# Optimization experiments

Hardware: AMD Instinct MI355X
Metric: run time of the kernel (lower is better)

The kernel has to match this reference:

```python
import jax, jax.numpy as jnp
import numpy as np

DK = 64
DROPOUT_P = 0.1


def setup_inputs() -> dict:
    key = jax.random.key(0)
    kq, kk, kv, km = jax.random.split(key, 4)
    B, S, D = 16, 2048, 64
    q = jax.random.normal(kq, (B, S, D), dtype=jnp.float32)
    k = jax.random.normal(kk, (B, S, D), dtype=jnp.float32)
    v = jax.random.normal(kv, (B, S, D), dtype=jnp.float32)
    attn_mask = jax.random.randint(km, (S, S), 0, 2, dtype=jnp.int32)
    return {"q": q, "k": k, "v": v, "attn_mask": attn_mask}


def reference(q, k, v, attn_mask):
    # q = q / sqrt(dk)
    qs = q * (1.0 / np.sqrt(DK)).astype(np.float32)
    # dots: [B, S_q, S_k]
    dots = jnp.einsum("bqd,bkd->bqk", qs, k)
    # mask: 0 -> -inf, 1 -> 0 (additive)
    add_mask = jnp.where(attn_mask == 0, -jnp.inf, 0.0).astype(dots.dtype)
    dots = dots + add_mask  # broadcast [S,S] over batch
    attn = jax.nn.softmax(dots, axis=-1)
    # inverted dropout, train mode, fixed key for determinism
    keep = jax.random.bernoulli(jax.random.key(42), 1.0 - DROPOUT_P, attn.shape)
    attn = jnp.where(keep, attn * (1.0 / (1.0 - DROPOUT_P)), 0.0)
    out = jnp.einsum("bqk,bkd->bqd", attn, v)
    return out
```

## Files before the change

### kernel.cpp

```cpp
#include <hip/hip_runtime.h>

#define BATCH 16
#define SEQ   2048
#define DIM   64
#define NTHREADS 256

typedef short bf16x8 __attribute__((ext_vector_type(8)));
typedef float f32x4 __attribute__((ext_vector_type(4)));

__device__ __forceinline__ int ldsoff(int row) {
  return row * 72 + 16 * (row >> 2);
}
#define LDS_SZ (64 * 72 + 16 * 16)

__device__ __forceinline__ unsigned tf_bits(unsigned f) {
  unsigned x0 = 0u;
  unsigned x1 = f;
  const unsigned ks1 = 42u;
  const unsigned ks2 = 0x1BD11BDAu ^ 42u;
  x1 += ks1;
#define TF_R(r) { x0 += x1; x1 = __builtin_amdgcn_alignbit(x1, x1, 32u - (r)); x1 ^= x0; }
  TF_R(13) TF_R(15) TF_R(26) TF_R(6)
  x0 += ks1; x1 += ks2 + 1u;
  TF_R(17) TF_R(29) TF_R(16) TF_R(24)
  x0 += ks2; x1 += 2u;
  TF_R(13) TF_R(15) TF_R(26) TF_R(6)
  x1 += ks1 + 3u;
  TF_R(17) TF_R(29) TF_R(16) TF_R(24)
  x0 += ks1; x1 += ks2 + 4u;
  TF_R(13) TF_R(15) TF_R(26) TF_R(6)
  x0 += ks2; x1 += 5u;
#undef TF_R
  return x0 ^ x1;
}
#define KEEP_THRESH 0xE6666600u

__device__ __forceinline__ unsigned pack_bf16x2(float lo, float hi) {
  const unsigned l = (__float_as_uint(lo) + 0x8000u) >> 16;
  const unsigned h = (__float_as_uint(hi) + 0x8000u) & 0xFFFF0000u;
  return h | l;
}
__device__ __forceinline__ unsigned pack_trunc(float lo, float hi) {
  return __builtin_amdgcn_perm(__float_as_uint(hi), __float_as_uint(lo), 0x07060302u);
}
__device__ __forceinline__ unsigned cvtpk(float lo, float hi) {
  unsigned r;
  asm("v_cvt_pk_bf16_f32 %0, %1, %2" : "=v"(r) : "v"(lo), "v"(hi));
  return r;
}

#define WS_KF 0
#define WS_VF 1048576
#define WS_MB 2097152
#define WS_O0 2228224
#define WS_L  4325376

__global__ __launch_bounds__(NTHREADS)
void prep(const float* __restrict__ k, const float* __restrict__ v,
          const int* __restrict__ mask, unsigned* __restrict__ ws) {
  __shared__ float TS[64 * 68];
  const int t = threadIdx.x;
  const unsigned bx = blockIdx.x;

  if (bx < 1024) {
    const int x  = (int)bx & 7;
    const int j  = (int)bx >> 3;
    const int b  = 2 * x + (j & 1);
    const int j2 = j >> 1;
    const int kt = j2 & 31;
    const int kv = j2 >> 5;
    const float* src = (kv ? v : k) + ((size_t)b * SEQ + kt * 64) * DIM;

#pragma unroll
    for (int s = 0; s < 4; ++s) {
      const int row = s * 16 + (t >> 4);
      const int c4  = (t & 15) * 4;
      *(float4*)&TS[row * 68 + c4] = *(const float4*)(src + (size_t)row * DIM + c4);
    }
    __syncthreads();

    const int lane = t & 63, tx = lane & 15, quad = lane >> 4, sub = t >> 6;
    if (kv == 0) {
#pragma unroll
      for (int i = 0; i < 2; ++i) {
        const int combo = sub * 2 + i, nt = combo >> 1, ks = combo & 1;
        const float* rp = &TS[(4 * tx + nt) * 68 + ks * 32 + quad * 8];
        const float4 f0 = *(const float4*)rp;
        const float4 f1 = *(const float4*)(rp + 4);
        uint4 wout;
        wout.x = cvtpk(f0.x, f0.y); wout.y = cvtpk(f0.z, f0.w);
        wout.z = cvtpk(f1.x, f1.y); wout.w = cvtpk(f1.z, f1.w);
        const unsigned e = ((((unsigned)b * 32 + kt) * 4 + nt) * 2 + ks) * 64 + lane;
        *(uint4*)(ws + WS_KF + (size_t)e * 4) = wout;
      }
    } else {
#pragma unroll
      for (int i = 0; i < 2; ++i) {
        const int combo = sub * 2 + i, nt = combo >> 1, ks = combo & 1;
        const float* cp = &TS[(ks * 32 + quad * 8) * 68 + nt * 16 + tx];
        uint4 wout;
        wout.x = cvtpk(cp[0 * 68], cp[1 * 68]);
        wout.y = cvtpk(cp[2 * 68], cp[3 * 68]);
        wout.z = cvtpk(cp[4 * 68], cp[5 * 68]);
        wout.w = cvtpk(cp[6 * 68], cp[7 * 68]);
        const unsigned e = ((((unsigned)b * 32 + kt) * 4 + nt) * 2 + ks) * 64 + lane;
        *(uint4*)(ws + WS_VF + (size_t)e * 4) = wout;
      }
    }
    return;
  }

  const unsigned pid = (bx - 1024u) * NTHREADS + (unsigned)t;
  const unsigned C4 = pid & 511u, R4 = pid >> 9;
  unsigned m16 = 0u;
#pragma unroll
  for (int rr = 0; rr < 4; ++rr) {
    const int4 mv = *(const int4*)(mask + (size_t)(4 * R4 + rr) * SEQ + 4 * C4);
    m16 |= (mv.x ? 1u : 0u) << (rr * 4 + 0);
    m16 |= (mv.y ? 1u : 0u) << (rr * 4 + 1);
    m16 |= (mv.z ? 1u : 0u) << (rr * 4 + 2);
    m16 |= (mv.w ? 1u : 0u) << (rr * 4 + 3);
  }
  ((unsigned short*)(ws + WS_MB))[pid] = (unsigned short)m16;
}

__global__ __launch_bounds__(NTHREADS, 4)
void attn_fwd(const float* __restrict__ q, const unsigned* __restrict__ ws,
              float* __restrict__ out) {
  __shared__ unsigned short PS[LDS_SZ];

  const int t    = threadIdx.x;
  const int w    = t >> 6;
  const int lane = t & 63;
  const int tx   = lane & 15;
  const int quad = lane >> 4;

  const int x  = (int)blockIdx.x & 7;
  const int j  = (int)blockIdx.x >> 3;
  const int bb = 2 * x + (j & 1);
  const int j2 = j >> 1;
  const int q0 = (j2 & 31) * 64;
  const int sk = j2 >> 5;
  const int qw = q0 + 16 * w;
  const int kt0 = sk * 16;

  const float qscale = 0.125f * 1.44269504088896340736f;

  bf16x8 aq[2];
  {
    const float* qr = q + ((size_t)bb * SEQ + qw + tx) * DIM + quad * 8;
#pragma unroll
    for (int ks = 0; ks < 2; ++ks) {
      const float4 f0 = *(const float4*)(qr + ks * 32);
      const float4 f1 = *(const float4*)(qr + ks * 32 + 4);
      union { unsigned u[4]; bf16x8 v; } a;
      a.u[0] = pack_bf16x2(f0.x * qscale, f0.y * qscale);
      a.u[1] = pack_bf16x2(f0.z * qscale, f0.w * qscale);
      a.u[2] = pack_bf16x2(f1.x * qscale, f1.y * qscale);
      a.u[3] = pack_bf16x2(f1.z * qscale, f1.w * qscale);
      aq[ks] = a.v;
    }
  }

  float lrun[4] = {0.f, 0.f, 0.f, 0.f};
  f32x4 oacc[4];
#pragma unroll
  for (int nt = 0; nt < 4; ++nt) oacc[nt] = (f32x4){0.f, 0.f, 0.f, 0.f};

  const unsigned* kfb = ws + WS_KF + (size_t)(bb * 32) * 2048 + (size_t)lane * 4;
  const unsigned* vfb = ws + WS_VF + (size_t)(bb * 32) * 2048 + (size_t)lane * 4;
  const unsigned short* maskp = (const unsigned short*)(ws + WS_MB)
      + ((size_t)((qw >> 2) + quad)) * 512 + tx;
  const unsigned fbase0 = (unsigned)(bb * SEQ + qw + quad * 4) * (unsigned)SEQ
                          + (unsigned)(4 * tx);

  bf16x8 vf[4][2];

#define RNG_PWRITE(kt_, qk_, mw_)                                              \
  {                                                                            \
    const unsigned fb = fbase0 + (unsigned)((kt_) * 64);                       \
    _Pragma("unroll")                                                          \
    for (int reg = 0; reg < 4; ++reg) {                                        \
      const unsigned mnib = (mw_) >> (reg * 4);                                \
      float pd[4];                                                             \
      float ls = 0.0f;                                                         \
      _Pragma("unroll")                                                        \
      for (int nt = 0; nt < 4; ++nt) {                                         \
        const float s = (mnib & (1u << nt)) ? qk_[nt][reg] : -1e30f;           \
        const float e = __builtin_amdgcn_exp2f(s);                             \
        ls += e;                                                               \
        const unsigned bits = tf_bits(fb + (unsigned)(reg * SEQ) + (unsigned)nt); \
        pd[nt] = (bits < KEEP_THRESH) ? e : 0.0f;                              \
      }                                                                        \
      lrun[reg] += ls;                                                         \
      uint2 pw;                                                                \
      pw.x = pack_trunc(pd[0], pd[1]);                                         \
      pw.y = pack_trunc(pd[2], pd[3]);                                         \
      *(uint2*)&PS[ldsoff(16 * w + quad * 4 + reg) + 4 * tx] = pw;             \
    }                                                                          \
  }

#define LOAD_KF(kt_)                                                           \
    const unsigned* kfp = kfb + (size_t)(kt_) * 2048;                          \
    bf16x8 kf[4][2];                                                           \
    _Pragma("unroll")                                                          \
    for (int nt = 0; nt < 4; ++nt)                                             \
      _Pragma("unroll")                                                        \
      for (int ks = 0; ks < 2; ++ks)                                           \
        kf[nt][ks] = *(const bf16x8*)(kfp + (nt * 2 + ks) * 256);

#define PV_STEP                                                                \
    _Pragma("unroll")                                                          \
    for (int ks = 0; ks < 2; ++ks) {                                           \
      const bf16x8 ap = *(const bf16x8*)&PS[ldsoff(16 * w + tx) + ks * 32 + quad * 8]; \
      _Pragma("unroll")                                                        \
      for (int nt = 0; nt < 4; ++nt)                                           \
        oacc[nt] = __builtin_amdgcn_mfma_f32_16x16x32_bf16(ap, vf[nt][ks],     \
                                                           oacc[nt], 0, 0, 0); \
    }

#define LOAD_VF(kt_)                                                           \
    const unsigned* vfp = vfb + (size_t)(kt_) * 2048;                          \
    _Pragma("unroll")                                                          \
    for (int nt = 0; nt < 4; ++nt)                                             \
      _Pragma("unroll")                                                        \
      for (int ks = 0; ks < 2; ++ks)                                           \
        vf[nt][ks] = *(const bf16x8*)(vfp + (nt * 2 + ks) * 256);

#define QK_STEP(qk_)                                                           \
    f32x4 qk_[4];                                                              \
    _Pragma("unroll")                                                          \
    for (int nt = 0; nt < 4; ++nt) {                                           \
      f32x4 c = (f32x4){0.f, 0.f, 0.f, 0.f};                                   \
      _Pragma("unroll")                                                        \
      for (int ks = 0; ks < 2; ++ks)                                           \
        c = __builtin_amdgcn_mfma_f32_16x16x32_bf16(aq[ks], kf[nt][ks], c, 0, 0, 0); \
      qk_[nt] = c;                                                             \
    }

  {
    LOAD_KF(kt0)
    LOAD_VF(kt0)
    const unsigned mwv = maskp[kt0 * 16];
    QK_STEP(qk)
    RNG_PWRITE(kt0, qk, mwv)
  }
#pragma unroll 1
  for (int kt = kt0 + 1; kt < kt0 + 16; ++kt) {
    LOAD_KF(kt)
    const unsigned mwv = maskp[kt * 16];
    PV_STEP
    LOAD_VF(kt)
    QK_STEP(qk)
    RNG_PWRITE(kt, qk, mwv)
  }
  PV_STEP

  float lsum[4];
#pragma unroll
  for (int reg = 0; reg < 4; ++reg) {
    float ls = lrun[reg];
    ls += __shfl_xor(ls, 1);
    ls += __shfl_xor(ls, 2);
    ls += __shfl_xor(ls, 4);
    ls += __shfl_xor(ls, 8);
    lsum[reg] = ls;
  }
  float* wsf = (float*)ws;
  const size_t off = ((size_t)bb * SEQ + qw) * DIM;
  float* ob = sk ? out + off : wsf + WS_O0 + off;
#pragma unroll
  for (int nt = 0; nt < 4; ++nt)
#pragma unroll
    for (int reg = 0; reg < 4; ++reg)
      ob[(size_t)(quad * 4 + reg) * DIM + nt * 16 + tx] = oacc[nt][reg];
  if (tx == 0) {
    float* lp = wsf + WS_L + sk * 32768 + bb * SEQ + qw + quad * 4;
#pragma unroll
    for (int reg = 0; reg < 4; ++reg) lp[reg] = lsum[reg];
  }
}

__global__ __launch_bounds__(NTHREADS)
void combine(float* __restrict__ out, const unsigned* __restrict__ ws) {
  const unsigned gid = blockIdx.x * NTHREADS + threadIdx.x;
  const float* wsf = (const float*)ws;
  const float4 a = ((const float4*)out)[gid];
  const float4 b = ((const float4*)(wsf + WS_O0))[gid];
  const unsigned row = gid >> 4;
  const float linv = (1.0f / 0.9f) / (wsf[WS_L + row] + wsf[WS_L + 32768u + row]);
  float4 o;
  o.x = (a.x + b.x) * linv;
  o.y = (a.y + b.y) * linv;
  o.z = (a.z + b.z) * linv;
  o.w = (a.w + b.w) * linv;
  ((float4*)out)[gid] = o;
}

extern "C" void kernel_launch(void* const* d_in, const int* in_sizes, int n_in,
                              void* d_out, int out_size, void* d_ws, size_t ws_size,
                              hipStream_t stream) {
  const float* q = (const float*)d_in[0];
  const float* k = (const float*)d_in[1];
  const float* v = (const float*)d_in[2];
  const int* mask = (const int*)d_in[3];
  float* out = (float*)d_out;
  unsigned* ws = (unsigned*)d_ws;

  hipLaunchKernelGGL(prep, dim3(2048), dim3(NTHREADS), 0, stream,
                     k, v, mask, ws);
  hipLaunchKernelGGL(attn_fwd, dim3(1024), dim3(NTHREADS), 0, stream,
                     q, ws, out);
  hipLaunchKernelGGL(combine, dim3(2048), dim3(NTHREADS), 0, stream, out, ws);
}
```

Measured before the change: 225.7 us.

## Fuse prep and combine into single attention kernel with in-block split-K reduction

```diff
diff --git a/kernel.cpp b/kernel.cpp
--- a/kernel.cpp
+++ b/kernel.cpp
@@ -49,100 +49,26 @@
   return r;
 }
 
-#define WS_KF 0
-#define WS_VF 1048576
-#define WS_MB 2097152
-#define WS_O0 2228224
-#define WS_L  4325376
-
-__global__ __launch_bounds__(NTHREADS)
-void prep(const float* __restrict__ k, const float* __restrict__ v,
-          const int* __restrict__ mask, unsigned* __restrict__ ws) {
-  __shared__ float TS[64 * 68];
-  const int t = threadIdx.x;
-  const unsigned bx = blockIdx.x;
-
-  if (bx < 1024) {
-    const int x  = (int)bx & 7;
-    const int j  = (int)bx >> 3;
-    const int b  = 2 * x + (j & 1);
-    const int j2 = j >> 1;
-    const int kt = j2 & 31;
-    const int kv = j2 >> 5;
-    const float* src = (kv ? v : k) + ((size_t)b * SEQ + kt * 64) * DIM;
-
-#pragma unroll
-    for (int s = 0; s < 4; ++s) {
-      const int row = s * 16 + (t >> 4);
-      const int c4  = (t & 15) * 4;
-      *(float4*)&TS[row * 68 + c4] = *(const float4*)(src + (size_t)row * DIM + c4);
-    }
-    __syncthreads();
-
-    const int lane = t & 63, tx = lane & 15, quad = lane >> 4, sub = t >> 6;
-    if (kv == 0) {
-#pragma unroll
-      for (int i = 0; i < 2; ++i) {
-        const int combo = sub * 2 + i, nt = combo >> 1, ks = combo & 1;
-        const float* rp = &TS[(4 * tx + nt) * 68 + ks * 32 + quad * 8];
-        const float4 f0 = *(const float4*)rp;
-        const float4 f1 = *(const float4*)(rp + 4);
-        uint4 wout;
-        wout.x = cvtpk(f0.x, f0.y); wout.y = cvtpk(f0.z, f0.w);
-        wout.z = cvtpk(f1.x, f1.y); wout.w = cvtpk(f1.z, f1.w);
-        const unsigned e = ((((unsigned)b * 32 + kt) * 4 + nt) * 2 + ks) * 64 + lane;
-        *(uint4*)(ws + WS_KF + (size_t)e * 4) = wout;
-      }
-    } else {
-#pragma unroll
-      for (int i = 0; i < 2; ++i) {
-        const int combo = sub * 2 + i, nt = combo >> 1, ks = combo & 1;
-        const float* cp = &TS[(ks * 32 + quad * 8) * 68 + nt * 16 + tx];
-        uint4 wout;
-        wout.x = cvtpk(cp[0 * 68], cp[1 * 68]);
-        wout.y = cvtpk(cp[2 * 68], cp[3 * 68]);
-        wout.z = cvtpk(cp[4 * 68], cp[5 * 68]);
-        wout.w = cvtpk(cp[6 * 68], cp[7 * 68]);
-        const unsigned e = ((((unsigned)b * 32 + kt) * 4 + nt) * 2 + ks) * 64 + lane;
-        *(uint4*)(ws + WS_VF + (size_t)e * 4) = wout;
-      }
-    }
-    return;
-  }
-
-  const unsigned pid = (bx - 1024u) * NTHREADS + (unsigned)t;
-  const unsigned C4 = pid & 511u, R4 = pid >> 9;
-  unsigned m16 = 0u;
-#pragma unroll
-  for (int rr = 0; rr < 4; ++rr) {
-    const int4 mv = *(const int4*)(mask + (size_t)(4 * R4 + rr) * SEQ + 4 * C4);
-    m16 |= (mv.x ? 1u : 0u) << (rr * 4 + 0);
-    m16 |= (mv.y ? 1u : 0u) << (rr * 4 + 1);
-    m16 |= (mv.z ? 1u : 0u) << (rr * 4 + 2);
-    m16 |= (mv.w ? 1u : 0u) << (rr * 4 + 3);
-  }
-  ((unsigned short*)(ws + WS_MB))[pid] = (unsigned short)m16;
-}
-
 __global__ __launch_bounds__(NTHREADS, 4)
-void attn_fwd(const float* __restrict__ q, const unsigned* __restrict__ ws,
+void attn_all(const float* __restrict__ q, const float* __restrict__ k,
+              const float* __restrict__ v, const int* __restrict__ mask,
               float* __restrict__ out) {
-  __shared__ unsigned short PS[LDS_SZ];
+  __shared__ __align__(16) unsigned short PS[LDS_SZ];
 
   const int t    = threadIdx.x;
   const int w    = t >> 6;
   const int lane = t & 63;
   const int tx   = lane & 15;
   const int quad = lane >> 4;
+  const int rh   = w & 1;
+  const int kh   = w >> 1;
 
   const int x  = (int)blockIdx.x & 7;
   const int j  = (int)blockIdx.x >> 3;
   const int bb = 2 * x + (j & 1);
-  const int j2 = j >> 1;
-  const int q0 = (j2 & 31) * 64;
-  const int sk = j2 >> 5;
-  const int qw = q0 + 16 * w;
-  const int kt0 = sk * 16;
+  const int qb = (j >> 1) * 32;
+  const int qw = qb + 16 * rh;
+  const int kt0 = kh * 16;
 
   const float qscale = 0.125f * 1.44269504088896340736f;
 
@@ -167,26 +93,83 @@
 #pragma unroll
   for (int nt = 0; nt < 4; ++nt) oacc[nt] = (f32x4){0.f, 0.f, 0.f, 0.f};
 
-  const unsigned* kfb = ws + WS_KF + (size_t)(bb * 32) * 2048 + (size_t)lane * 4;
-  const unsigned* vfb = ws + WS_VF + (size_t)(bb * 32) * 2048 + (size_t)lane * 4;
-  const unsigned short* maskp = (const unsigned short*)(ws + WS_MB)
-      + ((size_t)((qw >> 2) + quad)) * 512 + tx;
+  const float* kb = k + (size_t)bb * SEQ * DIM;
+  const float* vb = v + (size_t)bb * SEQ * DIM;
+  const int* mrow = mask + (size_t)(qw + quad * 4) * SEQ + 4 * tx;
   const unsigned fbase0 = (unsigned)(bb * SEQ + qw + quad * 4) * (unsigned)SEQ
                           + (unsigned)(4 * tx);
 
   bf16x8 vf[4][2];
 
-#define RNG_PWRITE(kt_, qk_, mw_)                                              \
+#define LOAD_KF(kt_)                                                           \
+    bf16x8 kf[4][2];                                                           \
+    _Pragma("unroll")                                                          \
+    for (int nt = 0; nt < 4; ++nt)                                             \
+      _Pragma("unroll")                                                        \
+      for (int ks = 0; ks < 2; ++ks) {                                         \
+        const float* rp = kb + (size_t)((kt_) * 64 + 4 * tx + nt) * DIM        \
+                             + ks * 32 + quad * 8;                             \
+        const float4 f0 = *(const float4*)rp;                                  \
+        const float4 f1 = *(const float4*)(rp + 4);                            \
+        union { unsigned u[4]; bf16x8 v; } c;                                  \
+        c.u[0] = cvtpk(f0.x, f0.y); c.u[1] = cvtpk(f0.z, f0.w);                \
+        c.u[2] = cvtpk(f1.x, f1.y); c.u[3] = cvtpk(f1.z, f1.w);                \
+        kf[nt][ks] = c.v;                                                      \
+      }
+
+#define LOAD_VF(kt_)                                                           \
+    _Pragma("unroll")                                                          \
+    for (int nt = 0; nt < 4; ++nt)                                             \
+      _Pragma("unroll")                                                        \
+      for (int ks = 0; ks < 2; ++ks) {                                         \
+        const float* cp = vb + (size_t)((kt_) * 64 + ks * 32 + quad * 8) * DIM \
+                             + nt * 16 + tx;                                   \
+        union { unsigned u[4]; bf16x8 v; } c;                                  \
+        c.u[0] = cvtpk(cp[0 * DIM], cp[1 * DIM]);                              \
+        c.u[1] = cvtpk(cp[2 * DIM], cp[3 * DIM]);                              \
+        c.u[2] = cvtpk(cp[4 * DIM], cp[5 * DIM]);                              \
+        c.u[3] = cvtpk(cp[6 * DIM], cp[7 * DIM]);                              \
+        vf[nt][ks] = c.v;                                                      \
+      }
+
+#define LOAD_MASK(kt_, mv_)                                                    \
+    int4 mv_[4];                                                               \
+    _Pragma("unroll")                                                          \
+    for (int reg = 0; reg < 4; ++reg)                                          \
+      mv_[reg] = *(const int4*)(mrow + (size_t)reg * SEQ + (kt_) * 64);
+
+#define PV_STEP                                                                \
+    _Pragma("unroll")                                                          \
+    for (int ks = 0; ks < 2; ++ks) {                                           \
+      const bf16x8 ap = *(const bf16x8*)&PS[ldsoff(16 * w + tx) + ks * 32 + quad * 8]; \
+      _Pragma("unroll")                                                        \
+      for (int nt = 0; nt < 4; ++nt)                                           \
+        oacc[nt] = __builtin_amdgcn_mfma_f32_16x16x32_bf16(ap, vf[nt][ks],     \
+                                                           oacc[nt], 0, 0, 0); \
+    }
+
+#define QK_STEP(qk_)                                                           \
+    f32x4 qk_[4];                                                              \
+    _Pragma("unroll")                                                          \
+    for (int nt = 0; nt < 4; ++nt) {                                           \
+      f32x4 c = (f32x4){0.f, 0.f, 0.f, 0.f};                                   \
+      _Pragma("unroll")                                                        \
+      for (int ks = 0; ks < 2; ++ks)                                           \
+        c = __builtin_amdgcn_mfma_f32_16x16x32_bf16(aq[ks], kf[nt][ks], c, 0, 0, 0); \
+      qk_[nt] = c;                                                             \
+    }
+
+#define RNG_PWRITE(kt_, qk_, mv_)                                              \
   {                                                                            \
     const unsigned fb = fbase0 + (unsigned)((kt_) * 64);                       \
     _Pragma("unroll")                                                          \
     for (int reg = 0; reg < 4; ++reg) {                                        \
-      const unsigned mnib = (mw_) >> (reg * 4);                                \
+      const int* mr = (const int*)&mv_[reg];                                   \
       float pd[4];                                                             \
       float ls = 0.0f;                                                         \
       _Pragma("unroll")                                                        \
       for (int nt = 0; nt < 4; ++nt) {                                         \
-        const float s = (mnib & (1u << nt)) ? qk_[nt][reg] : -1e30f;           \
+        const float s = mr[nt] ? qk_[nt][reg] : -1e30f;                        \
         const float e = __builtin_amdgcn_exp2f(s);                             \
         ls += e;                                                               \
         const unsigned bits = tf_bits(fb + (unsigned)(reg * SEQ) + (unsigned)nt); \
@@ -200,59 +183,21 @@
     }                                                                          \
   }
 
-#define LOAD_KF(kt_)                                                           \
-    const unsigned* kfp = kfb + (size_t)(kt_) * 2048;                          \
-    bf16x8 kf[4][2];                                                           \
-    _Pragma("unroll")                                                          \
-    for (int nt = 0; nt < 4; ++nt)                                             \
-      _Pragma("unroll")                                                        \
-      for (int ks = 0; ks < 2; ++ks)                                           \
-        kf[nt][ks] = *(const bf16x8*)(kfp + (nt * 2 + ks) * 256);
-
-#define PV_STEP                                                                \
-    _Pragma("unroll")                                                          \
-    for (int ks = 0; ks < 2; ++ks) {                                           \
-      const bf16x8 ap = *(const bf16x8*)&PS[ldsoff(16 * w + tx) + ks * 32 + quad * 8]; \
-      _Pragma("unroll")                                                        \
-      for (int nt = 0; nt < 4; ++nt)                                           \
-        oacc[nt] = __builtin_amdgcn_mfma_f32_16x16x32_bf16(ap, vf[nt][ks],     \
-                                                           oacc[nt], 0, 0, 0); \
-    }
-
-#define LOAD_VF(kt_)                                                           \
-    const unsigned* vfp = vfb + (size_t)(kt_) * 2048;                          \
-    _Pragma("unroll")                                                          \
-    for (int nt = 0; nt < 4; ++nt)                                             \
-      _Pragma("unroll")                                                        \
-      for (int ks = 0; ks < 2; ++ks)                                           \
-        vf[nt][ks] = *(const bf16x8*)(vfp + (nt * 2 + ks) * 256);
-
-#define QK_STEP(qk_)                                                           \
-    f32x4 qk_[4];                                                              \
-    _Pragma("unroll")                                                          \
-    for (int nt = 0; nt < 4; ++nt) {                                           \
-      f32x4 c = (f32x4){0.f, 0.f, 0.f, 0.f};                                   \
-      _Pragma("unroll")                                                        \
-      for (int ks = 0; ks < 2; ++ks)                                           \
-        c = __builtin_amdgcn_mfma_f32_16x16x32_bf16(aq[ks], kf[nt][ks], c, 0, 0, 0); \
-      qk_[nt] = c;                                                             \
-    }
-
   {
     LOAD_KF(kt0)
     LOAD_VF(kt0)
-    const unsigned mwv = maskp[kt0 * 16];
+    LOAD_MASK(kt0, mv)
     QK_STEP(qk)
-    RNG_PWRITE(kt0, qk, mwv)
+    RNG_PWRITE(kt0, qk, mv)
   }
 #pragma unroll 1
   for (int kt = kt0 + 1; kt < kt0 + 16; ++kt) {
     LOAD_KF(kt)
-    const unsigned mwv = maskp[kt * 16];
+    LOAD_MASK(kt, mv)
     PV_STEP
     LOAD_VF(kt)
     QK_STEP(qk)
-    RNG_PWRITE(kt, qk, mwv)
+    RNG_PWRITE(kt, qk, mv)
   }
   PV_STEP
 
@@ -266,35 +211,37 @@
     ls += __shfl_xor(ls, 8);
     lsum[reg] = ls;
   }
-  float* wsf = (float*)ws;
-  const size_t off = ((size_t)bb * SEQ + qw) * DIM;
-  float* ob = sk ? out + off : wsf + WS_O0 + off;
-#pragma unroll
-  for (int nt = 0; nt < 4; ++nt)
+
+  __syncthreads();
+  float* MB = (float*)PS;
+  float* ML = MB + 2048;
+  if (kh == 1) {
+#pragma unroll
+    for (int nt = 0; nt < 4; ++nt)
+#pragma unroll
+      for (int reg = 0; reg < 4; ++reg)
+        MB[(16 * rh + quad * 4 + reg) * 64 + nt * 16 + tx] = oacc[nt][reg];
+    if (tx == 0) {
+#pragma unroll
+      for (int reg = 0; reg < 4; ++reg)
+        ML[16 * rh + quad * 4 + reg] = lsum[reg];
+    }
+  }
+  __syncthreads();
+  if (kh == 0) {
+    float linv[4];
 #pragma unroll
     for (int reg = 0; reg < 4; ++reg)
-      ob[(size_t)(quad * 4 + reg) * DIM + nt * 16 + tx] = oacc[nt][reg];
-  if (tx == 0) {
-    float* lp = wsf + WS_L + sk * 32768 + bb * SEQ + qw + quad * 4;
-#pragma unroll
-    for (int reg = 0; reg < 4; ++reg) lp[reg] = lsum[reg];
-  }
-}
-
-__global__ __launch_bounds__(NTHREADS)
-void combine(float* __restrict__ out, const unsigned* __restrict__ ws) {
-  const unsigned gid = blockIdx.x * NTHREADS + threadIdx.x;
-  const float* wsf = (const float*)ws;
-  const float4 a = ((const float4*)out)[gid];
-  const float4 b = ((const float4*)(wsf + WS_O0))[gid];
-  const unsigned row = gid >> 4;
-  const float linv = (1.0f / 0.9f) / (wsf[WS_L + row] + wsf[WS_L + 32768u + row]);
-  float4 o;
-  o.x = (a.x + b.x) * linv;
-  o.y = (a.y + b.y) * linv;
-  o.z = (a.z + b.z) * linv;
-  o.w = (a.w + b.w) * linv;
-  ((float4*)out)[gid] = o;
+      linv[reg] = (1.0f / 0.9f) / (lsum[reg] + ML[16 * rh + quad * 4 + reg]);
+    float* ob = out + ((size_t)bb * SEQ + qw) * DIM;
+#pragma unroll
+    for (int nt = 0; nt < 4; ++nt)
+#pragma unroll
+      for (int reg = 0; reg < 4; ++reg)
+        ob[(size_t)(quad * 4 + reg) * DIM + nt * 16 + tx] =
+            (oacc[nt][reg] + MB[(16 * rh + quad * 4 + reg) * 64 + nt * 16 + tx])
+            * linv[reg];
+  }
 }
 
 extern "C" void kernel_launch(void* const* d_in, const int* in_sizes, int n_in,
@@ -305,11 +252,8 @@
   const float* v = (const float*)d_in[2];
   const int* mask = (const int*)d_in[3];
   float* out = (float*)d_out;
-  unsigned* ws = (unsigned*)d_ws;
-
-  hipLaunchKernelGGL(prep, dim3(2048), dim3(NTHREADS), 0, stream,
-                     k, v, mask, ws);
-  hipLaunchKernelGGL(attn_fwd, dim3(1024), dim3(NTHREADS), 0, stream,
-                     q, ws, out);
-  hipLaunchKernelGGL(combine, dim3(2048), dim3(NTHREADS), 0, stream, out, ws);
-}
+  (void)d_ws; (void)ws_size;
+
+  hipLaunchKernelGGL(attn_all, dim3(1024), dim3(NTHREADS), 0, stream,
+                     q, k, v, mask, out);
+}
```

After: 296.8 us. 31.5% more time.

## Fuse split-K combine into attention kernel via intra-block LDS reduction

Applied to the files above, without the earlier changes.

```diff
diff --git a/kernel.cpp b/kernel.cpp
--- a/kernel.cpp
+++ b/kernel.cpp
@@ -52,8 +52,6 @@
 #define WS_KF 0
 #define WS_VF 1048576
 #define WS_MB 2097152
-#define WS_O0 2228224
-#define WS_L  4325376
 
 __global__ __launch_bounds__(NTHREADS)
 void prep(const float* __restrict__ k, const float* __restrict__ v,
@@ -127,22 +125,22 @@
 __global__ __launch_bounds__(NTHREADS, 4)
 void attn_fwd(const float* __restrict__ q, const unsigned* __restrict__ ws,
               float* __restrict__ out) {
-  __shared__ unsigned short PS[LDS_SZ];
+  __shared__ __align__(16) unsigned short PS[LDS_SZ];
 
   const int t    = threadIdx.x;
   const int w    = t >> 6;
   const int lane = t & 63;
   const int tx   = lane & 15;
   const int quad = lane >> 4;
+  const int rh   = w & 1;
+  const int kh   = w >> 1;
 
   const int x  = (int)blockIdx.x & 7;
   const int j  = (int)blockIdx.x >> 3;
   const int bb = 2 * x + (j & 1);
-  const int j2 = j >> 1;
-  const int q0 = (j2 & 31) * 64;
-  const int sk = j2 >> 5;
-  const int qw = q0 + 16 * w;
-  const int kt0 = sk * 16;
+  const int qb = (j >> 1) * 32;
+  const int qw = qb + 16 * rh;
+  const int kt0 = kh * 16;
 
   const float qscale = 0.125f * 1.44269504088896340736f;
 
@@ -266,35 +264,37 @@
     ls += __shfl_xor(ls, 8);
     lsum[reg] = ls;
   }
-  float* wsf = (float*)ws;
-  const size_t off = ((size_t)bb * SEQ + qw) * DIM;
-  float* ob = sk ? out + off : wsf + WS_O0 + off;
-#pragma unroll
-  for (int nt = 0; nt < 4; ++nt)
+
+  __syncthreads();
+  float* MB = (float*)PS;
+  float* ML = MB + 2048;
+  if (kh == 1) {
+#pragma unroll
+    for (int nt = 0; nt < 4; ++nt)
+#pragma unroll
+      for (int reg = 0; reg < 4; ++reg)
+        MB[(16 * rh + quad * 4 + reg) * 64 + nt * 16 + tx] = oacc[nt][reg];
+    if (tx == 0) {
+#pragma unroll
+      for (int reg = 0; reg < 4; ++reg)
+        ML[16 * rh + quad * 4 + reg] = lsum[reg];
+    }
+  }
+  __syncthreads();
+  if (kh == 0) {
+    float linv[4];
 #pragma unroll
     for (int reg = 0; reg < 4; ++reg)
-      ob[(size_t)(quad * 4 + reg) * DIM + nt * 16 + tx] = oacc[nt][reg];
-  if (tx == 0) {
-    float* lp = wsf + WS_L + sk * 32768 + bb * SEQ + qw + quad * 4;
-#pragma unroll
-    for (int reg = 0; reg < 4; ++reg) lp[reg] = lsum[reg];
-  }
-}
-
-__global__ __launch_bounds__(NTHREADS)
-void combine(float* __restrict__ out, const unsigned* __restrict__ ws) {
-  const unsigned gid = blockIdx.x * NTHREADS + threadIdx.x;
-  const float* wsf = (const float*)ws;
-  const float4 a = ((const float4*)out)[gid];
-  const float4 b = ((const float4*)(wsf + WS_O0))[gid];
-  const unsigned row = gid >> 4;
-  const float linv = (1.0f / 0.9f) / (wsf[WS_L + row] + wsf[WS_L + 32768u + row]);
-  float4 o;
-  o.x = (a.x + b.x) * linv;
-  o.y = (a.y + b.y) * linv;
-  o.z = (a.z + b.z) * linv;
-  o.w = (a.w + b.w) * linv;
-  ((float4*)out)[gid] = o;
+      linv[reg] = (1.0f / 0.9f) / (lsum[reg] + ML[16 * rh + quad * 4 + reg]);
+    float* ob = out + ((size_t)bb * SEQ + qw) * DIM;
+#pragma unroll
+    for (int nt = 0; nt < 4; ++nt)
+#pragma unroll
+      for (int reg = 0; reg < 4; ++reg)
+        ob[(size_t)(quad * 4 + reg) * DIM + nt * 16 + tx] =
+            (oacc[nt][reg] + MB[(16 * rh + quad * 4 + reg) * 64 + nt * 16 + tx])
+            * linv[reg];
+  }
 }
 
 extern "C" void kernel_launch(void* const* d_in, const int* in_sizes, int n_in,
@@ -311,5 +311,4 @@
                      k, v, mask, ws);
   hipLaunchKernelGGL(attn_fwd, dim3(1024), dim3(NTHREADS), 0, stream,
                      q, ws, out);
-  hipLaunchKernelGGL(combine, dim3(2048), dim3(NTHREADS), 0, stream, out, ws);
-}
+}
```

New measurement: 220.3 us. 1.02x faster.
